# Kernel optimization log

Measured on AMD Instinct MI355X. Metric: run time of the kernel, lower is better.

Reference implementation:

```python
import jax, jax.numpy as jnp
import numpy as np

B, S, D = 4, 2048, 512
H = 8
DEPTH = D // H  # 64


def setup_inputs() -> dict:
    key = jax.random.key(0)
    ks = jax.random.split(key, 6)
    scale = 1.0 / np.sqrt(D)
    return {
        "x": jax.random.normal(ks[0], (B, S, D), dtype=jnp.float32),
        "y": jax.random.normal(ks[1], (B, S, D), dtype=jnp.float32),
        "W_q": jax.random.normal(ks[2], (D, D), dtype=jnp.float32) * scale,
        "W_k": jax.random.normal(ks[3], (D, D), dtype=jnp.float32) * scale,
        "W_v": jax.random.normal(ks[4], (D, D), dtype=jnp.float32) * scale,
        "W_o": jax.random.normal(ks[5], (D, D), dtype=jnp.float32) * scale,
    }


def _split_heads(t):
    # [B, S, D] -> [B, H, S, DEPTH]
    b, s, _ = t.shape
    return t.reshape(b, s, H, DEPTH).transpose(0, 2, 1, 3)


def reference(x, y, W_q, W_k, W_v, W_o):
    q = _split_heads(x @ W_q) * (DEPTH ** -0.5)   # [B,H,Sq,d]
    k = _split_heads(y @ W_k)                      # [B,H,Sk,d]
    v = _split_heads(y @ W_v)                      # [B,H,Sk,d]
    logits = jnp.einsum("bhqd,bhkd->bhqk", q, k)   # [B,H,Sq,Sk]
    weights = jax.nn.softmax(logits, axis=-1)
    attn = jnp.einsum("bhqk,bhkd->bhqd", weights, v)  # [B,H,Sq,d]
    attn = attn.transpose(0, 2, 1, 3).reshape(x.shape[0], x.shape[1], D)
    return attn @ W_o
```

## Files before the change

kernel.cpp:

```cpp
#include <hip/hip_runtime.h>
#include <hip/hip_bf16.h>
#include <math.h>
#include <stdint.h>

#define NB 4
#define NS 2048
#define ND 512
#define NH 8
#define DEP 64

typedef __attribute__((ext_vector_type(8))) short bf16x8;
typedef __attribute__((ext_vector_type(4))) short bf16x4;
typedef __attribute__((ext_vector_type(4))) float f32x4;

#define QSCALE 0.18033688011112042f

__device__ __forceinline__ short f2b(float f) {
  unsigned u = __float_as_uint(f);
  u += 0x7FFF + ((u >> 16) & 1);
  return (short)(u >> 16);
}
__device__ __forceinline__ unsigned pk2(float a, float b) {
  union { __hip_bfloat162 h; unsigned u; } c;
  c.h = __float22bfloat162_rn(float2{a, b});
  return c.u;
}
__device__ __forceinline__ void dma16(const void* g, void* l) {
  __builtin_amdgcn_global_load_lds(
      (const __attribute__((address_space(1))) void*)g,
      (__attribute__((address_space(3))) void*)l, 16, 0, 0);
}

__global__ __launch_bounds__(256) void cast_xy(const float* __restrict__ x,
                                               const float* __restrict__ y,
                                               short* __restrict__ xb,
                                               short* __restrict__ yb) {
  const float* src = blockIdx.y ? y : x;
  short* dst = blockIdx.y ? yb : xb;
  size_t i = ((size_t)blockIdx.x * 256 + threadIdx.x) * 4;
  float4 v = *(const float4*)(src + i);
  bf16x4 o;
  o[0] = f2b(v.x); o[1] = f2b(v.y); o[2] = f2b(v.z); o[3] = f2b(v.w);
  *(bf16x4*)(dst + i) = o;
}

__global__ __launch_bounds__(256) void trans_w(
    const float* __restrict__ W0, const float* __restrict__ W1,
    const float* __restrict__ W2, const float* __restrict__ W3,
    short* __restrict__ T0, short* __restrict__ T1, short* __restrict__ T2,
    short* __restrict__ T3) {
  const float* W = blockIdx.z == 0 ? W0 : blockIdx.z == 1 ? W1
                   : blockIdx.z == 2 ? W2 : W3;
  short* T = blockIdx.z == 0 ? T0 : blockIdx.z == 1 ? T1
             : blockIdx.z == 2 ? T2 : T3;
  __shared__ float tile[64][65];
  const int t = threadIdx.x;
  const int k0 = blockIdx.x * 64, n0 = blockIdx.y * 64;
#pragma unroll
  for (int i = 0; i < 4; ++i) {
    int r = (t >> 4) + i * 16;
    int c = (t & 15) * 4;
    float4 v = *(const float4*)&W[(size_t)(k0 + r) * ND + n0 + c];
    tile[r][c] = v.x; tile[r][c + 1] = v.y;
    tile[r][c + 2] = v.z; tile[r][c + 3] = v.w;
  }
  __syncthreads();
#pragma unroll
  for (int i = 0; i < 4; ++i) {
    int n = (t >> 4) + i * 16;
    int kc = (t & 15) * 4;
    bf16x4 o;
#pragma unroll
    for (int j = 0; j < 4; ++j) o[j] = f2b(tile[kc + j][n]);
    *(bf16x4*)&T[(size_t)(n0 + n) * ND + k0 + kc] = o;
  }
}

__device__ __forceinline__ void gemm_core(const short* __restrict__ A,
                                          const short* __restrict__ Bt,
                                          void* __restrict__ Cout, int mode,
                                          float alpha) {
  __shared__ short As[2][128 * 64];
  __shared__ short Bs[2][64 * 64];
  const int t = threadIdx.x;
  const int wave = t >> 6, lane = t & 63;
  const int m = lane & 15, quad = lane >> 4;
  const int m0 = blockIdx.y * 128, n0 = blockIdx.x * 64;
  const int mh = (wave >> 1) * 64, nh = (wave & 1) * 32;
  const int r8 = lane >> 3;
  const int c8 = (lane & 7) ^ r8;
  const int mx7 = m & 7;
  f32x4 acc[4][2];
#pragma unroll
  for (int i = 0; i < 4; ++i)
#pragma unroll
    for (int j = 0; j < 2; ++j) acc[i][j] = (f32x4){0.f, 0.f, 0.f, 0.f};

#pragma unroll
  for (int i = 0; i < 4; ++i)
    dma16(A + (size_t)(m0 + i * 32 + wave * 8 + r8) * ND + c8 * 8,
          As[0] + (i * 256 + wave * 64) * 8);
#pragma unroll
  for (int i = 0; i < 2; ++i)
    dma16(Bt + (size_t)(n0 + i * 32 + wave * 8 + r8) * ND + c8 * 8,
          Bs[0] + (i * 256 + wave * 64) * 8);

  int buf = 0;
  for (int k0 = 0; k0 < ND; k0 += 64, buf ^= 1) {
    __syncthreads();
    if (k0 + 64 < ND) {
#pragma unroll
      for (int i = 0; i < 4; ++i)
        dma16(A + (size_t)(m0 + i * 32 + wave * 8 + r8) * ND + k0 + 64 + c8 * 8,
              As[buf ^ 1] + (i * 256 + wave * 64) * 8);
#pragma unroll
      for (int i = 0; i < 2; ++i)
        dma16(Bt + (size_t)(n0 + i * 32 + wave * 8 + r8) * ND + k0 + 64 +
                  c8 * 8,
              Bs[buf ^ 1] + (i * 256 + wave * 64) * 8);
    }
    bf16x8 af[4][2], bf[2][2];
#pragma unroll
    for (int mt = 0; mt < 4; ++mt)
#pragma unroll
      for (int kc = 0; kc < 2; ++kc)
        af[mt][kc] = *(const bf16x8*)(As[buf] + (mh + mt * 16 + m) * 64 +
                                      ((kc * 4 + quad) ^ mx7) * 8);
#pragma unroll
    for (int nt = 0; nt < 2; ++nt)
#pragma unroll
      for (int kc = 0; kc < 2; ++kc)
        bf[nt][kc] = *(const bf16x8*)(Bs[buf] + (nh + nt * 16 + m) * 64 +
                                      ((kc * 4 + quad) ^ mx7) * 8);
#pragma unroll
    for (int mt = 0; mt < 4; ++mt)
#pragma unroll
      for (int nt = 0; nt < 2; ++nt)
#pragma unroll
        for (int kc = 0; kc < 2; ++kc)
          acc[mt][nt] = __builtin_amdgcn_mfma_f32_16x16x32_bf16(
              af[mt][kc], bf[nt][kc], acc[mt][nt], 0, 0, 0);
  }
  if (mode == 2) {
#pragma unroll
    for (int mt = 0; mt < 4; ++mt)
#pragma unroll
      for (int nt = 0; nt < 2; ++nt) {
        int row0 = m0 + mh + mt * 16 + quad * 4;
        int col = n0 + nh + nt * 16 + m;
        int b_ = row0 >> 11, s_ = row0 & (NS - 1);
        int h_ = col >> 6, d_ = col & (DEP - 1);
        uint2 p;
        p.x = pk2(acc[mt][nt][0] * alpha, acc[mt][nt][1] * alpha);
        p.y = pk2(acc[mt][nt][2] * alpha, acc[mt][nt][3] * alpha);
        *(uint2*)((short*)Cout +
                  (size_t)((b_ * NH + h_) * DEP + d_) * NS + s_) = p;
      }
  } else {
#pragma unroll
    for (int mt = 0; mt < 4; ++mt)
#pragma unroll
      for (int nt = 0; nt < 2; ++nt)
#pragma unroll
        for (int r = 0; r < 4; ++r) {
          int row = m0 + mh + mt * 16 + quad * 4 + r;
          int col = n0 + nh + nt * 16 + m;
          float v = acc[mt][nt][r] * alpha;
          if (mode == 1)
            ((short*)Cout)[(size_t)row * ND + col] = f2b(v);
          else
            ((float*)Cout)[(size_t)row * ND + col] = v;
        }
  }
}

__global__ __launch_bounds__(256) void qkv_gemm(
    const short* __restrict__ xb, const short* __restrict__ yb,
    const short* __restrict__ Wqt, const short* __restrict__ Wkt,
    const short* __restrict__ Wvt, short* __restrict__ Qb,
    short* __restrict__ Kb, short* __restrict__ Vtb) {
  if (blockIdx.z == 0)
    gemm_core(xb, Wqt, Qb, 1, QSCALE);
  else if (blockIdx.z == 1)
    gemm_core(yb, Wkt, Kb, 1, 1.0f);
  else
    gemm_core(yb, Wvt, Vtb, 2, 1.0f);
}

__global__ __launch_bounds__(256) void out_gemm(const short* __restrict__ Ab,
                                                const short* __restrict__ Wot,
                                                float* __restrict__ out) {
  gemm_core(Ab, Wot, out, 0, 1.0f);
}

__global__ __launch_bounds__(256) void attn_mfma(const short* __restrict__ Qb,
                                                 const short* __restrict__ Kb,
                                                 const short* __restrict__ Vtb,
                                                 short* __restrict__ Ob) {
  __shared__ short Ks[2][64 * 64];
  __shared__ short Vts[2][64 * 64];
  __shared__ short Pt[64 * 64];
  const int t = threadIdx.x;
  const int wave = t >> 6, lane = t & 63;
  const int m = lane & 15, quad = lane >> 4;
  const int bh = blockIdx.y, b = bh >> 3, h = bh & 7;
  const int q0 = blockIdx.x * 64;
  const int wq = wave * 16;
  const size_t rowb = (size_t)b * NS;
  const short* Vtbase = Vtb + (size_t)(bh * DEP) * NS;
  const int r8 = lane >> 3;
  const int c8 = (lane & 7) ^ r8;
  const int mx7 = m & 7;

  bf16x8 qf[2];
#pragma unroll
  for (int kc = 0; kc < 2; ++kc)
    qf[kc] = *(const bf16x8*)(Qb + (rowb + q0 + wq + m) * ND + h * DEP +
                              kc * 32 + quad * 8);

  float l_ = 0.0f;
  f32x4 Ot[4];
#pragma unroll
  for (int mt = 0; mt < 4; ++mt) Ot[mt] = (f32x4){0.f, 0.f, 0.f, 0.f};

#pragma unroll
  for (int i = 0; i < 2; ++i) {
    int row = i * 32 + wave * 8 + r8;
    dma16(Kb + (rowb + row) * ND + h * DEP + c8 * 8,
          Ks[0] + (i * 256 + wave * 64) * 8);
    dma16(Vtbase + (size_t)row * NS + c8 * 8,
          Vts[0] + (i * 256 + wave * 64) * 8);
  }

  int buf = 0;
  for (int kv0 = 0; kv0 < NS; kv0 += 64, buf ^= 1) {
    __syncthreads();
    if (kv0 + 64 < NS) {
#pragma unroll
      for (int i = 0; i < 2; ++i) {
        int row = i * 32 + wave * 8 + r8;
        dma16(Kb + (rowb + kv0 + 64 + row) * ND + h * DEP + c8 * 8,
              Ks[buf ^ 1] + (i * 256 + wave * 64) * 8);
        dma16(Vtbase + (size_t)row * NS + kv0 + 64 + c8 * 8,
              Vts[buf ^ 1] + (i * 256 + wave * 64) * 8);
      }
    }

    f32x4 St[4];
#pragma unroll
    for (int mt = 0; mt < 4; ++mt) St[mt] = (f32x4){0.f, 0.f, 0.f, 0.f};
#pragma unroll
    for (int mt = 0; mt < 4; ++mt)
#pragma unroll
      for (int kc = 0; kc < 2; ++kc) {
        bf16x8 kf = *(const bf16x8*)(Ks[buf] + (mt * 16 + m) * 64 +
                                     ((kc * 4 + quad) ^ mx7) * 8);
        St[mt] = __builtin_amdgcn_mfma_f32_16x16x32_bf16(kf, qf[kc], St[mt],
                                                         0, 0, 0);
      }

    float rs = 0.0f;
#pragma unroll
    for (int mt = 0; mt < 4; ++mt) {
      float p0 = __builtin_amdgcn_exp2f(St[mt][0]);
      float p1 = __builtin_amdgcn_exp2f(St[mt][1]);
      float p2 = __builtin_amdgcn_exp2f(St[mt][2]);
      float p3 = __builtin_amdgcn_exp2f(St[mt][3]);
      rs += (p0 + p1) + (p2 + p3);
      uint2 pk;
      pk.x = pk2(p0, p1);
      pk.y = pk2(p2, p3);
      *(uint2*)(Pt + (wq + m) * 64 + ((mt * 2 + (quad >> 1)) ^ mx7) * 8 +
                (quad & 1) * 4) = pk;
    }
    l_ += rs;

#pragma unroll
    for (int kc = 0; kc < 2; ++kc) {
      bf16x8 pf = *(const bf16x8*)(Pt + (wq + m) * 64 +
                                   ((kc * 4 + quad) ^ mx7) * 8);
#pragma unroll
      for (int mt = 0; mt < 4; ++mt) {
        bf16x8 vf = *(const bf16x8*)(Vts[buf] + (mt * 16 + m) * 64 +
                                     ((kc * 4 + quad) ^ mx7) * 8);
        Ot[mt] = __builtin_amdgcn_mfma_f32_16x16x32_bf16(vf, pf, Ot[mt],
                                                         0, 0, 0);
      }
    }
  }

  l_ += __shfl_xor(l_, 16, 64);
  l_ += __shfl_xor(l_, 32, 64);
  float linv = 1.0f / l_;
  size_t row = rowb + q0 + wq + m;
#pragma unroll
  for (int mt = 0; mt < 4; ++mt)
#pragma unroll
    for (int r = 0; r < 4; ++r)
      Ob[row * ND + h * DEP + mt * 16 + quad * 4 + r] = f2b(Ot[mt][r] * linv);
}

extern "C" void kernel_launch(void* const* d_in, const int* in_sizes, int n_in,
                              void* d_out, int out_size, void* d_ws,
                              size_t ws_size, hipStream_t stream) {
  const float* x = (const float*)d_in[0];
  const float* y = (const float*)d_in[1];
  const float* Wq = (const float*)d_in[2];
  const float* Wk = (const float*)d_in[3];
  const float* Wv = (const float*)d_in[4];
  const float* Wo = (const float*)d_in[5];
  float* out = (float*)d_out;

  const size_t mat = (size_t)NB * NS * ND;
  const size_t wsz = (size_t)ND * ND;
  short* xb = (short*)d_ws;
  short* yb = xb + mat;
  short* Wqt = yb + mat;
  short* Wkt = Wqt + wsz;
  short* Wvt = Wkt + wsz;
  short* Wot = Wvt + wsz;
  short* Qb = Wot + wsz;
  short* Kb = Qb + mat;
  short* Vtb = Kb + mat;
  short* attnb = xb;

  cast_xy<<<dim3(mat / 1024, 2), 256, 0, stream>>>(x, y, xb, yb);
  trans_w<<<dim3(8, 8, 4), 256, 0, stream>>>(Wq, Wk, Wv, Wo, Wqt, Wkt, Wvt,
                                             Wot);
  qkv_gemm<<<dim3(ND / 64, (NB * NS) / 128, 3), 256, 0, stream>>>(
      xb, yb, Wqt, Wkt, Wvt, Qb, Kb, Vtb);
  attn_mfma<<<dim3(NS / 64, NB * NH), 256, 0, stream>>>(Qb, Kb, Vtb, attnb);
  out_gemm<<<dim3(ND / 64, (NB * NS) / 128), 256, 0, stream>>>(attnb, Wot,
                                                               out);
}
```

Measured before the change: 192.2 us.

## Merge cast and weight transpose kernels; widen QKV GEMM tile to 128x128

Merges the input cast and weight transpose into one prep launch, using extra grid rows for the transpose blocks. Replaces the QKV projection GEMM with a 128x128 tile variant, single-buffered in LDS, where each wave computes a 64x64 sub-tile. This raises operand reuse per LDS load and halves the QKV grid, at the cost of losing the double-buffered overlap and using more accumulator registers. Out GEMM keeps the old 128x64 double-buffered path. The prep grid launches many idle blocks for the transpose row (only 256 of 8192 do work).

```diff
diff --git a/kernel.cpp b/kernel.cpp
--- a/kernel.cpp
+++ b/kernel.cpp
@@ -31,31 +31,30 @@
       (__attribute__((address_space(3))) void*)l, 16, 0, 0);
 }
 
-__global__ __launch_bounds__(256) void cast_xy(const float* __restrict__ x,
-                                               const float* __restrict__ y,
-                                               short* __restrict__ xb,
-                                               short* __restrict__ yb) {
-  const float* src = blockIdx.y ? y : x;
-  short* dst = blockIdx.y ? yb : xb;
-  size_t i = ((size_t)blockIdx.x * 256 + threadIdx.x) * 4;
-  float4 v = *(const float4*)(src + i);
-  bf16x4 o;
-  o[0] = f2b(v.x); o[1] = f2b(v.y); o[2] = f2b(v.z); o[3] = f2b(v.w);
-  *(bf16x4*)(dst + i) = o;
-}
-
-__global__ __launch_bounds__(256) void trans_w(
+__global__ __launch_bounds__(256) void prep(
+    const float* __restrict__ x, const float* __restrict__ y,
     const float* __restrict__ W0, const float* __restrict__ W1,
     const float* __restrict__ W2, const float* __restrict__ W3,
-    short* __restrict__ T0, short* __restrict__ T1, short* __restrict__ T2,
-    short* __restrict__ T3) {
-  const float* W = blockIdx.z == 0 ? W0 : blockIdx.z == 1 ? W1
-                   : blockIdx.z == 2 ? W2 : W3;
-  short* T = blockIdx.z == 0 ? T0 : blockIdx.z == 1 ? T1
-             : blockIdx.z == 2 ? T2 : T3;
+    short* __restrict__ xb, short* __restrict__ yb, short* __restrict__ T0,
+    short* __restrict__ T1, short* __restrict__ T2, short* __restrict__ T3) {
+  const int t = threadIdx.x;
+  if (blockIdx.y < 2) {
+    const float* src = blockIdx.y ? y : x;
+    short* dst = blockIdx.y ? yb : xb;
+    size_t i = ((size_t)blockIdx.x * 256 + t) * 4;
+    float4 v = *(const float4*)(src + i);
+    bf16x4 o;
+    o[0] = f2b(v.x); o[1] = f2b(v.y); o[2] = f2b(v.z); o[3] = f2b(v.w);
+    *(bf16x4*)(dst + i) = o;
+    return;
+  }
+  const int bx = blockIdx.x;
+  if (bx >= 256) return;
+  const int wj = bx >> 6, rem = bx & 63;
+  const float* W = wj == 0 ? W0 : wj == 1 ? W1 : wj == 2 ? W2 : W3;
+  short* T = wj == 0 ? T0 : wj == 1 ? T1 : wj == 2 ? T2 : T3;
   __shared__ float tile[64][65];
-  const int t = threadIdx.x;
-  const int k0 = blockIdx.x * 64, n0 = blockIdx.y * 64;
+  const int k0 = (rem >> 3) * 64, n0 = (rem & 7) * 64;
 #pragma unroll
   for (int i = 0; i < 4; ++i) {
     int r = (t >> 4) + i * 16;
@@ -76,10 +75,103 @@
   }
 }
 
-__device__ __forceinline__ void gemm_core(const short* __restrict__ A,
-                                          const short* __restrict__ Bt,
-                                          void* __restrict__ Cout, int mode,
-                                          float alpha) {
+__device__ __forceinline__ void gemm128(const short* __restrict__ A,
+                                        const short* __restrict__ Bt,
+                                        short* __restrict__ Cout, int mode,
+                                        float alpha) {
+  __shared__ short As[128 * 64];
+  __shared__ short Bs[128 * 64];
+  const int t = threadIdx.x;
+  const int wave = t >> 6, lane = t & 63;
+  const int m = lane & 15, quad = lane >> 4;
+  const int m0 = blockIdx.y * 128, n0 = blockIdx.x * 128;
+  const int mh = (wave >> 1) * 64, nh = (wave & 1) * 64;
+  const int r8 = lane >> 3;
+  const int c8 = (lane & 7) ^ r8;
+  const int mx7 = m & 7;
+  f32x4 acc[4][4];
+#pragma unroll
+  for (int i = 0; i < 4; ++i)
+#pragma unroll
+    for (int j = 0; j < 4; ++j) acc[i][j] = (f32x4){0.f, 0.f, 0.f, 0.f};
+
+  for (int k0 = 0; k0 < ND; k0 += 64) {
+    __syncthreads();
+#pragma unroll
+    for (int i = 0; i < 4; ++i) {
+      int row = i * 32 + wave * 8 + r8;
+      dma16(A + (size_t)(m0 + row) * ND + k0 + c8 * 8,
+            As + (i * 256 + wave * 64) * 8);
+      dma16(Bt + (size_t)(n0 + row) * ND + k0 + c8 * 8,
+            Bs + (i * 256 + wave * 64) * 8);
+    }
+    __syncthreads();
+    bf16x8 af[4][2], bf[4][2];
+#pragma unroll
+    for (int mt = 0; mt < 4; ++mt)
+#pragma unroll
+      for (int kc = 0; kc < 2; ++kc)
+        af[mt][kc] = *(const bf16x8*)(As + (mh + mt * 16 + m) * 64 +
+                                      ((kc * 4 + quad) ^ mx7) * 8);
+#pragma unroll
+    for (int nt = 0; nt < 4; ++nt)
+#pragma unroll
+      for (int kc = 0; kc < 2; ++kc)
+        bf[nt][kc] = *(const bf16x8*)(Bs + (nh + nt * 16 + m) * 64 +
+                                      ((kc * 4 + quad) ^ mx7) * 8);
+#pragma unroll
+    for (int mt = 0; mt < 4; ++mt)
+#pragma unroll
+      for (int nt = 0; nt < 4; ++nt)
+#pragma unroll
+        for (int kc = 0; kc < 2; ++kc)
+          acc[mt][nt] = __builtin_amdgcn_mfma_f32_16x16x32_bf16(
+              af[mt][kc], bf[nt][kc], acc[mt][nt], 0, 0, 0);
+  }
+  if (mode == 2) {
+#pragma unroll
+    for (int mt = 0; mt < 4; ++mt)
+#pragma unroll
+      for (int nt = 0; nt < 4; ++nt) {
+        int row0 = m0 + mh + mt * 16 + quad * 4;
+        int col = n0 + nh + nt * 16 + m;
+        int b_ = row0 >> 11, s_ = row0 & (NS - 1);
+        int h_ = col >> 6, d_ = col & (DEP - 1);
+        uint2 p;
+        p.x = pk2(acc[mt][nt][0] * alpha, acc[mt][nt][1] * alpha);
+        p.y = pk2(acc[mt][nt][2] * alpha, acc[mt][nt][3] * alpha);
+        *(uint2*)(Cout + (size_t)((b_ * NH + h_) * DEP + d_) * NS + s_) = p;
+      }
+  } else {
+#pragma unroll
+    for (int mt = 0; mt < 4; ++mt)
+#pragma unroll
+      for (int nt = 0; nt < 4; ++nt)
+#pragma unroll
+        for (int r = 0; r < 4; ++r) {
+          int row = m0 + mh + mt * 16 + quad * 4 + r;
+          int col = n0 + nh + nt * 16 + m;
+          Cout[(size_t)row * ND + col] = f2b(acc[mt][nt][r] * alpha);
+        }
+  }
+}
+
+__global__ __launch_bounds__(256) void qkv_gemm(
+    const short* __restrict__ xb, const short* __restrict__ yb,
+    const short* __restrict__ Wqt, const short* __restrict__ Wkt,
+    const short* __restrict__ Wvt, short* __restrict__ Qb,
+    short* __restrict__ Kb, short* __restrict__ Vtb) {
+  if (blockIdx.z == 0)
+    gemm128(xb, Wqt, Qb, 1, QSCALE);
+  else if (blockIdx.z == 1)
+    gemm128(yb, Wkt, Kb, 1, 1.0f);
+  else
+    gemm128(yb, Wvt, Vtb, 2, 1.0f);
+}
+
+__global__ __launch_bounds__(256) void out_gemm(const short* __restrict__ A,
+                                                const short* __restrict__ Bt,
+                                                float* __restrict__ Cout) {
   __shared__ short As[2][128 * 64];
   __shared__ short Bs[2][64 * 64];
   const int t = threadIdx.x;
@@ -141,56 +233,16 @@
           acc[mt][nt] = __builtin_amdgcn_mfma_f32_16x16x32_bf16(
               af[mt][kc], bf[nt][kc], acc[mt][nt], 0, 0, 0);
   }
-  if (mode == 2) {
-#pragma unroll
-    for (int mt = 0; mt < 4; ++mt)
-#pragma unroll
-      for (int nt = 0; nt < 2; ++nt) {
-        int row0 = m0 + mh + mt * 16 + quad * 4;
+#pragma unroll
+  for (int mt = 0; mt < 4; ++mt)
+#pragma unroll
+    for (int nt = 0; nt < 2; ++nt)
+#pragma unroll
+      for (int r = 0; r < 4; ++r) {
+        int row = m0 + mh + mt * 16 + quad * 4 + r;
         int col = n0 + nh + nt * 16 + m;
-        int b_ = row0 >> 11, s_ = row0 & (NS - 1);
-        int h_ = col >> 6, d_ = col & (DEP - 1);
-        uint2 p;
-        p.x = pk2(acc[mt][nt][0] * alpha, acc[mt][nt][1] * alpha);
-        p.y = pk2(acc[mt][nt][2] * alpha, acc[mt][nt][3] * alpha);
-        *(uint2*)((short*)Cout +
-                  (size_t)((b_ * NH + h_) * DEP + d_) * NS + s_) = p;
-      }
-  } else {
-#pragma unroll
-    for (int mt = 0; mt < 4; ++mt)
-#pragma unroll
-      for (int nt = 0; nt < 2; ++nt)
-#pragma unroll
-        for (int r = 0; r < 4; ++r) {
-          int row = m0 + mh + mt * 16 + quad * 4 + r;
-          int col = n0 + nh + nt * 16 + m;
-          float v = acc[mt][nt][r] * alpha;
-          if (mode == 1)
-            ((short*)Cout)[(size_t)row * ND + col] = f2b(v);
-          else
-            ((float*)Cout)[(size_t)row * ND + col] = v;
-        }
-  }
-}
-
-__global__ __launch_bounds__(256) void qkv_gemm(
-    const short* __restrict__ xb, const short* __restrict__ yb,
-    const short* __restrict__ Wqt, const short* __restrict__ Wkt,
-    const short* __restrict__ Wvt, short* __restrict__ Qb,
-    short* __restrict__ Kb, short* __restrict__ Vtb) {
-  if (blockIdx.z == 0)
-    gemm_core(xb, Wqt, Qb, 1, QSCALE);
-  else if (blockIdx.z == 1)
-    gemm_core(yb, Wkt, Kb, 1, 1.0f);
-  else
-    gemm_core(yb, Wvt, Vtb, 2, 1.0f);
-}
-
-__global__ __launch_bounds__(256) void out_gemm(const short* __restrict__ Ab,
-                                                const short* __restrict__ Wot,
-                                                float* __restrict__ out) {
-  gemm_core(Ab, Wot, out, 0, 1.0f);
+        Cout[(size_t)row * ND + col] = acc[mt][nt][r];
+      }
 }
 
 __global__ __launch_bounds__(256) void attn_mfma(const short* __restrict__ Qb,
@@ -324,10 +376,9 @@
   short* Vtb = Kb + mat;
   short* attnb = xb;
 
-  cast_xy<<<dim3(mat / 1024, 2), 256, 0, stream>>>(x, y, xb, yb);
-  trans_w<<<dim3(8, 8, 4), 256, 0, stream>>>(Wq, Wk, Wv, Wo, Wqt, Wkt, Wvt,
-                                             Wot);
-  qkv_gemm<<<dim3(ND / 64, (NB * NS) / 128, 3), 256, 0, stream>>>(
+  prep<<<dim3(mat / 1024, 3), 256, 0, stream>>>(x, y, Wq, Wk, Wv, Wo, xb, yb,
+                                                Wqt, Wkt, Wvt, Wot);
+  qkv_gemm<<<dim3(ND / 128, (NB * NS) / 128, 3), 256, 0, stream>>>(
       xb, yb, Wqt, Wkt, Wvt, Qb, Kb, Vtb);
   attn_mfma<<<dim3(NS / 64, NB * NH), 256, 0, stream>>>(Qb, Kb, Vtb, attnb);
   out_gemm<<<dim3(ND / 64, (NB * NS) / 128), 256, 0, stream>>>(attnb, Wot,
```

Measured after the change: 186.4 us. 3.0% less time.
